# Kernel tuning notes

Measured on AMD Instinct MI355X. Metric: run time of the kernel, lower is better.

## Reference

```python
import jax, jax.numpy as jnp
import numpy as np

N_ENT = 14951   # entities (FB15K-style multimodal KG)
N_REL = 1345    # relations == number of context sub-graphs
N_NODES = 120000  # nodes in the batched context graph (b_x length)
N_EDGES = 480000  # edges in the normalized batched adjacency


def _glorot(key, shape):
    scale = np.sqrt(2.0 / (shape[0] + shape[1])).astype(np.float32)
    return jax.random.normal(key, shape, dtype=jnp.float32) * scale


def setup_inputs() -> dict:
    key = jax.random.key(0)
    ks = jax.random.split(key, 16)
    inp = {}
    inp["img_feat"] = jax.random.normal(ks[0], (N_ENT, 4096), dtype=jnp.float32)
    inp["text_feat"] = jax.random.normal(ks[1], (N_ENT, 300), dtype=jnp.float32)
    inp["rel_emb"] = jax.random.normal(ks[2], (N_REL, 300), dtype=jnp.float32)
    # learned parameters (eval mode: dropout = identity)
    inp["W_img_text"] = _glorot(ks[3], (4396, 100)); inp["b_img_text"] = jnp.zeros((100,), jnp.float32)
    inp["W_rel_input"] = _glorot(ks[4], (300, 100)); inp["b_rel_input"] = jnp.zeros((100,), jnp.float32)
    inp["W_gc1"] = _glorot(ks[5], (200, 256)); inp["b_gc1"] = jnp.zeros((256,), jnp.float32)
    inp["W_gc2"] = _glorot(ks[6], (256, 200)); inp["b_gc2"] = jnp.zeros((200,), jnp.float32)
    inp["W_emb"] = _glorot(ks[7], (400, 1)); inp["b_emb"] = jnp.zeros((1,), jnp.float32)
    inp["W_emb_out"] = _glorot(ks[8], (400, 200)); inp["b_emb_out"] = jnp.zeros((200,), jnp.float32)
    inp["W_rel"] = _glorot(ks[9], (300, 200)); inp["b_rel"] = jnp.zeros((200,), jnp.float32)
    # row-normalized adjacency of the batched context graph, as edge list
    inp["edge_weight"] = jax.random.uniform(ks[10], (N_EDGES,), dtype=jnp.float32)
    inp["b_x"] = jax.random.randint(ks[11], (N_NODES,), 0, N_ENT)
    inp["b_graph"] = jax.random.randint(ks[12], (N_NODES,), 0, N_REL)
    inp["edge_src"] = jax.random.randint(ks[13], (N_EDGES,), 0, N_NODES)
    inp["edge_dst"] = jax.random.randint(ks[14], (N_EDGES,), 0, N_NODES)
    return inp


def reference(img_feat, text_feat, rel_emb, W_img_text, b_img_text, W_rel_input,
              b_rel_input, W_gc1, b_gc1, W_gc2, b_gc2, W_emb, b_emb, W_emb_out,
              b_emb_out, W_rel, b_rel, edge_weight, b_x, b_graph, edge_src, edge_dst):
    seg_sum = lambda v, idx, n: jax.ops.segment_sum(v, idx, num_segments=n)

    def spmm(h):  # normalized adjacency @ h via edge-list gather/scatter
        return seg_sum(h[edge_src] * edge_weight[:, None], edge_dst, N_NODES)

    # multimodal entity encoder: Linear(4396 -> 100)
    emf = jnp.concatenate([img_feat, text_feat], axis=1) @ W_img_text + b_img_text
    # relation context encoder: Linear(300 -> 100) + ReLU
    rel_in = jax.nn.relu(rel_emb @ W_rel_input + b_rel_input)
    # batched context-graph node features [M, 200]
    h = jnp.concatenate([emf[b_x], rel_in[b_graph]], axis=1)
    # two-layer GCN encoder (SGCN1)
    h1 = jax.nn.relu(spmm(h @ W_gc1) + b_gc1)
    h2 = spmm(h1 @ W_gc2) + b_gc2          # [M, 200]
    # scatter_mean over entity ids, broadcast back
    cnt = seg_sum(jnp.ones((N_NODES,), h2.dtype), b_x, N_ENT)
    mean = seg_sum(h2, b_x, N_ENT) / jnp.maximum(cnt, 1.0)[:, None]
    emb = jnp.concatenate([h2, mean[b_x]], axis=1)   # [M, 400]
    score = emb @ W_emb + b_emb                      # [M, 1]
    # scatter_softmax over segments b_x (numerically stable)
    smax = jax.ops.segment_max(score, b_x, num_segments=N_ENT)
    e = jnp.exp(score - smax[b_x])
    z_s = e / seg_sum(e, b_x, N_ENT)[b_x]
    new_out = seg_sum(z_s * emb, b_x, N_ENT) @ W_emb_out + b_emb_out  # [N_ENT, 200]
    # relation output encoder: Linear(300 -> 200) + ReLU
    rel_context = jax.nn.relu(rel_emb @ W_rel + b_rel)                # [N_REL, 200]
    return new_out, rel_context
```

## Files before the change

kernel.cpp:

```cpp
#include <hip/hip_runtime.h>

#define N_ENT 14951
#define N_REL 1345
#define NNODE 120000
#define NEDGE 480000
#define MP_ENC 14976
#define KP_ENC 4480
#define NP_ENC 112

static inline int ceil_div(int a, int b){ return (a + b - 1) / b; }

typedef __bf16 bf16x8 __attribute__((ext_vector_type(8)));
typedef float f32x4 __attribute__((ext_vector_type(4)));

__device__ inline unsigned short f2bf(float f){
  unsigned u = __float_as_uint(f);
  return (unsigned short)((u + 0x7fffu + ((u >> 16) & 1u)) >> 16);
}

__global__ __launch_bounds__(256) void enc_mfma(
    const float* __restrict__ img, const float* __restrict__ txt,
    const unsigned short* __restrict__ Wt1, float* __restrict__ part)
{
  __shared__ unsigned short As[64 * 40];
  __shared__ unsigned short Bs[112 * 40];
  const int t = threadIdx.x;
  const int m0 = blockIdx.x * 64;
  const int s = blockIdx.y;
  const int l = t & 63, w = t >> 6;
  f32x4 acc[7];
  #pragma unroll
  for (int i = 0; i < 7; i++) acc[i] = f32x4{0.f, 0.f, 0.f, 0.f};

  for (int step = 0; step < 35; ++step) {
    const int kb = s * 1120 + step * 32;
    #pragma unroll
    for (int p = 0; p < 2; ++p) {
      const int c = t + p * 256;
      const int row = c >> 3, kq = c & 7;
      const int rowg = m0 + row;
      const int k = kb + kq * 4;
      float4 v = make_float4(0.f, 0.f, 0.f, 0.f);
      if (rowg < N_ENT) {
        if (k < 4096)      v = *(const float4*)(img + (size_t)rowg * 4096 + k);
        else if (k < 4396) v = *(const float4*)(txt + (size_t)rowg * 300 + (k - 4096));
      }
      ushort4 b;
      b.x = f2bf(v.x); b.y = f2bf(v.y); b.z = f2bf(v.z); b.w = f2bf(v.w);
      *(ushort4*)&As[row * 40 + kq * 4] = b;
    }
    {
      const int n = t >> 2, k16 = t & 3;
      *(uint4*)&Bs[n * 40 + k16 * 8] = *(const uint4*)(Wt1 + (size_t)n * KP_ENC + kb + k16 * 8);
      if (t < 192) {
        const int c = t + 256;
        const int n2 = c >> 2, k2 = c & 3;
        *(uint4*)&Bs[n2 * 40 + k2 * 8] = *(const uint4*)(Wt1 + (size_t)n2 * KP_ENC + kb + k2 * 8);
      }
    }
    __syncthreads();
    bf16x8 a = *(const bf16x8*)&As[(w * 16 + (l & 15)) * 40 + (l >> 4) * 8];
    #pragma unroll
    for (int ct = 0; ct < 7; ++ct) {
      bf16x8 bb = *(const bf16x8*)&Bs[(ct * 16 + (l & 15)) * 40 + (l >> 4) * 8];
      acc[ct] = __builtin_amdgcn_mfma_f32_16x16x32_bf16(a, bb, acc[ct], 0, 0, 0);
    }
    __syncthreads();
  }
  const int rb = m0 + w * 16 + (l >> 4) * 4;
  const int col = l & 15;
  #pragma unroll
  for (int ct = 0; ct < 7; ++ct)
    #pragma unroll
    for (int i = 0; i < 4; ++i)
      part[((size_t)s * MP_ENC + rb + i) * NP_ENC + ct * 16 + col] = acc[ct][i];
}

__global__ __launch_bounds__(256) void enc_reduce(
    const float* __restrict__ part, const float* __restrict__ bias, float* __restrict__ emf)
{
  int i = blockIdx.x * 256 + threadIdx.x;
  if (i >= N_ENT * 100) return;
  int r = i / 100, c = i % 100;
  float v = bias[c];
  #pragma unroll
  for (int s = 0; s < 4; ++s) v += part[((size_t)s * MP_ENC + r) * NP_ENC + c];
  emf[(size_t)r * 100 + c] = v;
}

__global__ __launch_bounds__(256) void gemm2_mfma(
    const float* __restrict__ h1, const unsigned short* __restrict__ Wt2,
    float* __restrict__ hg2)
{
  __shared__ unsigned short As[64 * 40];
  __shared__ unsigned short Bs[208 * 40];
  const int t = threadIdx.x;
  const int m0 = blockIdx.x * 64;
  const int l = t & 63, w = t >> 6;
  f32x4 acc[13];
  #pragma unroll
  for (int i = 0; i < 13; i++) acc[i] = f32x4{0.f, 0.f, 0.f, 0.f};

  for (int step = 0; step < 8; ++step) {
    const int kb = step * 32;
    #pragma unroll
    for (int p = 0; p < 2; ++p) {
      const int c = t + p * 256;
      const int row = c >> 3, kq = c & 7;
      float4 v = *(const float4*)(h1 + (size_t)(m0 + row) * 256 + kb + kq * 4);
      ushort4 b;
      b.x = f2bf(v.x); b.y = f2bf(v.y); b.z = f2bf(v.z); b.w = f2bf(v.w);
      *(ushort4*)&As[row * 40 + kq * 4] = b;
    }
    #pragma unroll
    for (int p = 0; p < 4; ++p) {
      const int c = t + p * 256;
      if (c < 832) {
        const int n = c >> 2, k16 = c & 3;
        *(uint4*)&Bs[n * 40 + k16 * 8] = *(const uint4*)(Wt2 + (size_t)n * 256 + kb + k16 * 8);
      }
    }
    __syncthreads();
    bf16x8 a = *(const bf16x8*)&As[(w * 16 + (l & 15)) * 40 + (l >> 4) * 8];
    #pragma unroll
    for (int ct = 0; ct < 13; ++ct) {
      bf16x8 bb = *(const bf16x8*)&Bs[(ct * 16 + (l & 15)) * 40 + (l >> 4) * 8];
      acc[ct] = __builtin_amdgcn_mfma_f32_16x16x32_bf16(a, bb, acc[ct], 0, 0, 0);
    }
    __syncthreads();
  }
  const int rb = m0 + w * 16 + (l >> 4) * 4;
  const int col0 = l & 15;
  #pragma unroll
  for (int ct = 0; ct < 13; ++ct) {
    const int col = ct * 16 + col0;
    if (col < 200) {
      #pragma unroll
      for (int i = 0; i < 4; ++i)
        hg2[(size_t)(rb + i) * 200 + col] = acc[ct][i];
    }
  }
}

__global__ __launch_bounds__(256) void wt1_k(const float* __restrict__ W, unsigned short* __restrict__ Wt)
{
  int n = blockIdx.y;
  int k = blockIdx.x * 256 + threadIdx.x;
  if (k >= KP_ENC) return;
  float v = (n < 100 && k < 4396) ? W[(size_t)k * 100 + n] : 0.f;
  Wt[(size_t)n * KP_ENC + k] = f2bf(v);
}
__global__ __launch_bounds__(256) void wt2_k(const float* __restrict__ W, unsigned short* __restrict__ Wt)
{
  int i = blockIdx.x * 256 + threadIdx.x;
  if (i >= 208 * 256) return;
  int n = i >> 8, k = i & 255;
  float v = (n < 200) ? W[(size_t)k * 200 + n] : 0.f;
  Wt[i] = f2bf(v);
}

template<bool RELU, bool HASBIAS>
__global__ __launch_bounds__(256) void gemm_f32(
    const float* __restrict__ A1, int K1, const float* __restrict__ A2,
    const float* __restrict__ B, const float* __restrict__ bias,
    float* __restrict__ C, int M, int K, int N)
{
  constexpr int BM = 64, BN = 128, BK = 16;
  __shared__ float As[BK][BM + 4];
  __shared__ float Bs[BK][BN];
  const int t = threadIdx.x;
  const int m0 = blockIdx.y * BM, n0 = blockIdx.x * BN;
  const int tr = t >> 4, tc = t & 15;
  const int tm0 = tr * 4, tn0 = tc * 8;
  const int K2 = K - K1;
  const int arow = t >> 2, aq = (t & 3) * 4;
  const int brow = t >> 4, bc0 = (t & 15) * 4;
  float acc[4][8];
  #pragma unroll
  for (int i = 0; i < 4; i++)
    #pragma unroll
    for (int j = 0; j < 8; j++) acc[i][j] = 0.f;

  for (int k0 = 0; k0 < K; k0 += BK) {
    {
      const int r = m0 + arow;
      const int k = k0 + aq;
      float4 v = make_float4(0.f, 0.f, 0.f, 0.f);
      if (r < M) {
        if (k + 3 < K1) {
          v = *(const float4*)(A1 + (size_t)r * K1 + k);
        } else if (k >= K1 && (k - K1) + 3 < K2) {
          v = *(const float4*)(A2 + (size_t)r * K2 + (k - K1));
        } else {
          float tmp[4] = {0.f, 0.f, 0.f, 0.f};
          #pragma unroll
          for (int j = 0; j < 4; j++) {
            int kj = k + j;
            if (kj < K) tmp[j] = (kj < K1) ? A1[(size_t)r * K1 + kj]
                                           : A2[(size_t)r * K2 + (kj - K1)];
          }
          v = make_float4(tmp[0], tmp[1], tmp[2], tmp[3]);
        }
      }
      As[aq + 0][arow] = v.x; As[aq + 1][arow] = v.y;
      As[aq + 2][arow] = v.z; As[aq + 3][arow] = v.w;
    }
    {
      const int k = k0 + brow;
      #pragma unroll
      for (int h = 0; h < 2; h++) {
        const int n = n0 + bc0 + h * 64;
        float4 v = make_float4(0.f, 0.f, 0.f, 0.f);
        if (k < K) {
          if (n + 3 < N) {
            v = *(const float4*)(B + (size_t)k * N + n);
          } else {
            float tmp[4] = {0.f, 0.f, 0.f, 0.f};
            for (int j = 0; j < 4; j++) if (n + j < N) tmp[j] = B[(size_t)k * N + n + j];
            v = make_float4(tmp[0], tmp[1], tmp[2], tmp[3]);
          }
        }
        *(float4*)&Bs[brow][bc0 + h * 64] = v;
      }
    }
    __syncthreads();
    #pragma unroll
    for (int k = 0; k < BK; k++) {
      float a[4], b[8];
      *(float4*)&a[0] = *(const float4*)&As[k][tm0];
      *(float4*)&b[0] = *(const float4*)&Bs[k][tn0];
      *(float4*)&b[4] = *(const float4*)&Bs[k][tn0 + 4];
      #pragma unroll
      for (int i = 0; i < 4; i++)
        #pragma unroll
        for (int j = 0; j < 8; j++) acc[i][j] = fmaf(a[i], b[j], acc[i][j]);
    }
    __syncthreads();
  }
  #pragma unroll
  for (int i = 0; i < 4; i++) {
    const int r = m0 + tm0 + i;
    if (r >= M) continue;
    #pragma unroll
    for (int j = 0; j < 8; j++) {
      const int c = n0 + tn0 + j;
      if (c >= N) continue;
      float v = acc[i][j];
      if (HASBIAS) v += bias[c];
      if (RELU) v = fmaxf(v, 0.f);
      C[(size_t)r * N + c] = v;
    }
  }
}

__global__ __launch_bounds__(256) void hist_k(const int* __restrict__ idx, int* __restrict__ hist, int n)
{
  int i = blockIdx.x * blockDim.x + threadIdx.x;
  if (i < n) atomicAdd(&hist[idx[i]], 1);
}

__global__ __launch_bounds__(256) void scan1_k(const int* __restrict__ hist, int* __restrict__ base,
                                               int* __restrict__ partial, int n)
{
  __shared__ int s[256];
  const int t = threadIdx.x;
  const int i0 = blockIdx.x * 1024 + t * 4;
  int v[4];
  #pragma unroll
  for (int j = 0; j < 4; j++) v[j] = (i0 + j < n) ? hist[i0 + j] : 0;
  const int tsum = v[0] + v[1] + v[2] + v[3];
  s[t] = tsum;
  __syncthreads();
  #pragma unroll
  for (int off = 1; off < 256; off <<= 1) {
    int u = (t >= off) ? s[t - off] : 0;
    __syncthreads();
    s[t] += u;
    __syncthreads();
  }
  int run = s[t] - tsum;
  #pragma unroll
  for (int j = 0; j < 4; j++) {
    if (i0 + j < n) base[i0 + j] = run;
    run += v[j];
  }
  if (t == 255) partial[blockIdx.x] = s[255];
}

__global__ __launch_bounds__(256) void scan2_k(int* __restrict__ partial, int nb, int* __restrict__ total_dst)
{
  __shared__ int s[256];
  const int t = threadIdx.x;
  const int v = (t < nb) ? partial[t] : 0;
  s[t] = v;
  __syncthreads();
  #pragma unroll
  for (int off = 1; off < 256; off <<= 1) {
    int u = (t >= off) ? s[t - off] : 0;
    __syncthreads();
    s[t] += u;
    __syncthreads();
  }
  if (t < nb) partial[t] = s[t] - v;
  if (t == 255) *total_dst = s[255];
}

__global__ __launch_bounds__(256) void scan3_k(int* __restrict__ base, const int* __restrict__ partial, int n)
{
  int i = blockIdx.x * 256 + threadIdx.x;
  if (i < n) base[i] += partial[blockIdx.x >> 2];
}

__global__ __launch_bounds__(256) void edge_scatter_k(
    const int* __restrict__ esrc, const int* __restrict__ edst, const float* __restrict__ ew,
    const int* __restrict__ bx, const int* __restrict__ bg,
    const int* __restrict__ ebase, int* __restrict__ ecur,
    float* __restrict__ s_w, int* __restrict__ s_src,
    int* __restrict__ s_en, int* __restrict__ s_gn)
{
  int e = blockIdx.x * blockDim.x + threadIdx.x;
  if (e >= NEDGE) return;
  int d = edst[e];
  int p = ebase[d] + atomicAdd(&ecur[d], 1);
  int s = esrc[e];
  s_w[p] = ew[e];
  s_src[p] = s;
  s_en[p] = bx[s];
  s_gn[p] = bg[s];
}

__global__ __launch_bounds__(256) void node_scatter_k(
    const int* __restrict__ bx, const int* __restrict__ nbase, int* __restrict__ ncur,
    int* __restrict__ node_of)
{
  int i = blockIdx.x * blockDim.x + threadIdx.x;
  if (i >= NNODE) return;
  int ent = bx[i];
  int p = nbase[ent] + atomicAdd(&ncur[ent], 1);
  node_of[p] = i;
}

__global__ __launch_bounds__(256) void spmm1_g(
    const int* __restrict__ ebase, const float* __restrict__ s_w,
    const int* __restrict__ s_en, const int* __restrict__ s_gn,
    const float* __restrict__ eg1, const float* __restrict__ rg1,
    const float* __restrict__ b_g1, float* __restrict__ out)
{
  const int gid = blockIdx.x * blockDim.x + threadIdx.x;
  const int d = gid >> 6, lane = gid & 63;
  if (d >= NNODE) return;
  const int p0 = ebase[d], p1 = ebase[d + 1];
  float4 acc = make_float4(0.f, 0.f, 0.f, 0.f);
  for (int p = p0; p < p1; ++p) {
    const float w = s_w[p];
    const int en = s_en[p], gn = s_gn[p];
    const float4 v = ((const float4*)(eg1 + (size_t)en * 256))[lane];
    const float4 u = ((const float4*)(rg1 + (size_t)gn * 256))[lane];
    acc.x += w * (v.x + u.x); acc.y += w * (v.y + u.y);
    acc.z += w * (v.z + u.z); acc.w += w * (v.w + u.w);
  }
  const float4 b = ((const float4*)b_g1)[lane];
  acc.x = fmaxf(acc.x + b.x, 0.f); acc.y = fmaxf(acc.y + b.y, 0.f);
  acc.z = fmaxf(acc.z + b.z, 0.f); acc.w = fmaxf(acc.w + b.w, 0.f);
  ((float4*)(out + (size_t)d * 256))[lane] = acc;
}

__global__ __launch_bounds__(256) void spmm2_g(
    const int* __restrict__ ebase, const float* __restrict__ s_w,
    const int* __restrict__ s_src, const float* __restrict__ hg2,
    const float* __restrict__ b_g2, const float* __restrict__ W_e,
    float* __restrict__ h2, float* __restrict__ score)
{
  const int gid = blockIdx.x * blockDim.x + threadIdx.x;
  const int d = gid >> 6, lane = gid & 63;
  if (d >= NNODE) return;
  const int p0 = ebase[d], p1 = ebase[d + 1];
  float4 acc = make_float4(0.f, 0.f, 0.f, 0.f);
  if (lane < 50) {
    for (int p = p0; p < p1; ++p) {
      const float w = s_w[p];
      const int s = s_src[p];
      const float4 v = ((const float4*)(hg2 + (size_t)s * 200))[lane];
      acc.x += w * v.x; acc.y += w * v.y; acc.z += w * v.z; acc.w += w * v.w;
    }
    const float4 b = ((const float4*)b_g2)[lane];
    acc.x += b.x; acc.y += b.y; acc.z += b.z; acc.w += b.w;
    ((float4*)(h2 + (size_t)d * 200))[lane] = acc;
  }
  float s = 0.f;
  if (lane < 50) {
    const float4 we = ((const float4*)W_e)[lane];
    s = acc.x * we.x + acc.y * we.y + acc.z * we.z + acc.w * we.w;
  }
  for (int off = 32; off; off >>= 1) s += __shfl_down(s, off);
  if (lane == 0) score[d] = s;
}

__global__ __launch_bounds__(256) void ent_k(
    const int* __restrict__ nbase, const int* __restrict__ node_of,
    const float* __restrict__ h2, const float* __restrict__ score,
    float* __restrict__ embE)
{
  const int gid = blockIdx.x * blockDim.x + threadIdx.x;
  const int ent = gid >> 6, lane = gid & 63;
  if (ent >= N_ENT) return;
  const int p0 = nbase[ent], p1 = nbase[ent + 1];
  const int cnt = p1 - p0;
  float m = -3.4e38f;
  for (int p = p0 + lane; p < p1; p += 64) m = fmaxf(m, score[node_of[p]]);
  #pragma unroll
  for (int off = 32; off; off >>= 1) m = fmaxf(m, __shfl_xor(m, off));
  float es = 0.f;
  for (int p = p0 + lane; p < p1; p += 64) es += __expf(score[node_of[p]] - m);
  #pragma unroll
  for (int off = 32; off; off >>= 1) es += __shfl_xor(es, off);
  const float inv_es = (cnt > 0) ? 1.f / es : 0.f;
  const float inv_cnt = 1.f / fmaxf((float)cnt, 1.f);
  float4 aw = make_float4(0.f, 0.f, 0.f, 0.f);
  float4 am = make_float4(0.f, 0.f, 0.f, 0.f);
  for (int p = p0; p < p1; ++p) {
    const int nd = node_of[p];
    const float z = __expf(score[nd] - m) * inv_es;
    if (lane < 50) {
      const float4 v = ((const float4*)(h2 + (size_t)nd * 200))[lane];
      aw.x += z * v.x; aw.y += z * v.y; aw.z += z * v.z; aw.w += z * v.w;
      am.x += v.x; am.y += v.y; am.z += v.z; am.w += v.w;
    }
  }
  if (lane < 50) {
    ((float4*)(embE + (size_t)ent * 400))[lane] = aw;
    float4 mn = make_float4(am.x * inv_cnt, am.y * inv_cnt, am.z * inv_cnt, am.w * inv_cnt);
    ((float4*)(embE + (size_t)ent * 400 + 200))[lane] = mn;
  }
}

extern "C" void kernel_launch(void* const* d_in, const int* in_sizes, int n_in,
                              void* d_out, int out_size, void* d_ws, size_t ws_size,
                              hipStream_t stream)
{
  const float* img  = (const float*)d_in[0];
  const float* txt  = (const float*)d_in[1];
  const float* rel  = (const float*)d_in[2];
  const float* W_it = (const float*)d_in[3];
  const float* b_it = (const float*)d_in[4];
  const float* W_ri = (const float*)d_in[5];
  const float* b_ri = (const float*)d_in[6];
  const float* W_g1 = (const float*)d_in[7];
  const float* b_g1 = (const float*)d_in[8];
  const float* W_g2 = (const float*)d_in[9];
  const float* b_g2 = (const float*)d_in[10];
  const float* W_e  = (const float*)d_in[11];
  const float* W_eo = (const float*)d_in[13];
  const float* b_eo = (const float*)d_in[14];
  const float* W_r  = (const float*)d_in[15];
  const float* b_r  = (const float*)d_in[16];
  const float* ew   = (const float*)d_in[17];
  const int*   bx   = (const int*)d_in[18];
  const int*   bg   = (const int*)d_in[19];
  const int*   esrc = (const int*)d_in[20];
  const int*   edst = (const int*)d_in[21];

  float* ws = (float*)d_ws;
  size_t off = 0;
  auto alloc = [&](size_t n){ size_t r = off; off += (n + 255) & ~(size_t)255; return r; };
  float* emf  = ws + alloc((size_t)N_ENT * 100);
  float* rin  = ws + alloc((size_t)N_REL * 100);
  float* eg1  = ws + alloc((size_t)N_ENT * 256);
  float* rg1  = ws + alloc((size_t)N_REL * 256);
  float* big1 = ws + alloc((size_t)NNODE * 256);
  float* hg2  = ws + alloc((size_t)NNODE * 200);
  float* embE = ws + alloc((size_t)N_ENT * 400);
  float* score = ws + alloc(NNODE);
  int* ehist = (int*)(ws + alloc(NNODE));
  int* ecur  = (int*)(ws + alloc(NNODE));
  int* ebase = (int*)(ws + alloc(NNODE + 1));
  int* nhist = (int*)(ws + alloc(N_ENT));
  int* ncur  = (int*)(ws + alloc(N_ENT));
  int* nbase = (int*)(ws + alloc(N_ENT + 1));
  int* epart = (int*)(ws + alloc(256));
  int* npart = (int*)(ws + alloc(256));
  float* s_w  = ws + alloc(NEDGE);
  int* s_src  = (int*)(ws + alloc(NEDGE));
  int* s_en   = (int*)(ws + alloc(NEDGE));
  int* s_gn   = (int*)(ws + alloc(NEDGE));
  int* node_of = (int*)(ws + alloc(NNODE));
  unsigned short* Wt1 = (unsigned short*)(ws + alloc((size_t)NP_ENC * KP_ENC / 2));
  unsigned short* Wt2 = (unsigned short*)(ws + alloc((size_t)208 * 256 / 2));
  float* part = hg2;
  float* h2 = big1;

  dim3 blk(256);

  hipMemsetAsync(ehist, 0, (size_t)NNODE * 4, stream);
  hipMemsetAsync(ecur,  0, (size_t)NNODE * 4, stream);
  hipMemsetAsync(nhist, 0, (size_t)N_ENT * 4, stream);
  hipMemsetAsync(ncur,  0, (size_t)N_ENT * 4, stream);
  hist_k<<<ceil_div(NEDGE, 256), blk, 0, stream>>>(edst, ehist, NEDGE);
  hist_k<<<ceil_div(NNODE, 256), blk, 0, stream>>>(bx, nhist, NNODE);
  scan1_k<<<ceil_div(NNODE, 1024), blk, 0, stream>>>(ehist, ebase, epart, NNODE);
  scan2_k<<<1, blk, 0, stream>>>(epart, ceil_div(NNODE, 1024), ebase + NNODE);
  scan3_k<<<ceil_div(NNODE, 256), blk, 0, stream>>>(ebase, epart, NNODE);
  scan1_k<<<ceil_div(N_ENT, 1024), blk, 0, stream>>>(nhist, nbase, npart, N_ENT);
  scan2_k<<<1, blk, 0, stream>>>(npart, ceil_div(N_ENT, 1024), nbase + N_ENT);
  scan3_k<<<ceil_div(N_ENT, 256), blk, 0, stream>>>(nbase, npart, N_ENT);
  edge_scatter_k<<<ceil_div(NEDGE, 256), blk, 0, stream>>>(
      esrc, edst, ew, bx, bg, ebase, ecur, s_w, s_src, s_en, s_gn);
  node_scatter_k<<<ceil_div(NNODE, 256), blk, 0, stream>>>(bx, nbase, ncur, node_of);

  wt1_k<<<dim3(ceil_div(KP_ENC, 256), NP_ENC), blk, 0, stream>>>(W_it, Wt1);
  wt2_k<<<ceil_div(208 * 256, 256), blk, 0, stream>>>(W_g2, Wt2);

  enc_mfma<<<dim3(MP_ENC / 64, 4), blk, 0, stream>>>(img, txt, Wt1, part);
  enc_reduce<<<ceil_div(N_ENT * 100, 256), blk, 0, stream>>>(part, b_it, emf);

  gemm_f32<true, true><<<dim3(1, ceil_div(N_REL, 64)), blk, 0, stream>>>(
      rel, 300, rel, W_ri, b_ri, rin, N_REL, 300, 100);
  gemm_f32<false, false><<<dim3(2, ceil_div(N_ENT, 64)), blk, 0, stream>>>(
      emf, 100, emf, W_g1, nullptr, eg1, N_ENT, 100, 256);
  gemm_f32<false, false><<<dim3(2, ceil_div(N_REL, 64)), blk, 0, stream>>>(
      rin, 100, rin, W_g1 + 100 * 256, nullptr, rg1, N_REL, 100, 256);

  spmm1_g<<<ceil_div(NNODE * 64, 256), blk, 0, stream>>>(
      ebase, s_w, s_en, s_gn, eg1, rg1, b_g1, big1);

  gemm2_mfma<<<NNODE / 64, blk, 0, stream>>>(big1, Wt2, hg2);
  spmm2_g<<<ceil_div(NNODE * 64, 256), blk, 0, stream>>>(
      ebase, s_w, s_src, hg2, b_g2, W_e, h2, score);

  ent_k<<<ceil_div(N_ENT * 64, 256), blk, 0, stream>>>(nbase, node_of, h2, score, embE);

  float* out_new = (float*)d_out;
  float* out_rel = out_new + (size_t)N_ENT * 200;
  gemm_f32<false, true><<<dim3(2, ceil_div(N_ENT, 64)), blk, 0, stream>>>(
      embE, 400, embE, W_eo, b_eo, out_new, N_ENT, 400, 200);
  gemm_f32<true, true><<<dim3(2, ceil_div(N_REL, 64)), blk, 0, stream>>>(
      rel, 300, rel, W_r, b_r, out_rel, N_REL, 300, 200);
}
```

Before: 706.6 us.

## Reorder GCN layers to aggregate before transform and fuse score into GEMM

Both GCN layers now do the sparse neighbour aggregation first and the dense weight multiply second, instead of the reverse. Layer 1 gathers the narrow 100-wide entity and relation features and then runs a new bf16 MFMA GEMM with fused bias and ReLU. This replaces the fp32 per-entity GEMMs and the 512-float-per-edge gathers. Layer 2 gathers the 256-wide h1 rows and then runs the MFMA GEMM with fused bias and the attention-score dot product. The cost is a wider random gather in layer 2 and an extra full-size intermediate buffer, and layer-1 inputs are now rounded to bf16 after aggregation.

```diff
diff --git a/kernel.cpp b/kernel.cpp
--- a/kernel.cpp
+++ b/kernel.cpp
@@ -88,9 +88,61 @@
   emf[(size_t)r * 100 + c] = v;
 }
 
-__global__ __launch_bounds__(256) void gemm2_mfma(
-    const float* __restrict__ h1, const unsigned short* __restrict__ Wt2,
-    float* __restrict__ hg2)
+__global__ __launch_bounds__(256) void gemm1_mfma(
+    const float* __restrict__ hagg, const unsigned short* __restrict__ Wtg1,
+    const float* __restrict__ b_g1, float* __restrict__ h1)
+{
+  __shared__ unsigned short As[64 * 40];
+  __shared__ unsigned short Bs[256 * 40];
+  const int t = threadIdx.x;
+  const int m0 = blockIdx.x * 64;
+  const int l = t & 63, w = t >> 6;
+  f32x4 acc[16];
+  #pragma unroll
+  for (int i = 0; i < 16; i++) acc[i] = f32x4{0.f, 0.f, 0.f, 0.f};
+
+  for (int step = 0; step < 7; ++step) {
+    const int kb = step * 32;
+    #pragma unroll
+    for (int p = 0; p < 2; ++p) {
+      const int c = t + p * 256;
+      const int row = c >> 3, kq = c & 7;
+      float4 v = *(const float4*)(hagg + (size_t)(m0 + row) * 224 + kb + kq * 4);
+      ushort4 b;
+      b.x = f2bf(v.x); b.y = f2bf(v.y); b.z = f2bf(v.z); b.w = f2bf(v.w);
+      *(ushort4*)&As[row * 40 + kq * 4] = b;
+    }
+    #pragma unroll
+    for (int p = 0; p < 4; ++p) {
+      const int c = t + p * 256;
+      const int n = c >> 2, k16 = c & 3;
+      *(uint4*)&Bs[n * 40 + k16 * 8] = *(const uint4*)(Wtg1 + (size_t)n * 224 + kb + k16 * 8);
+    }
+    __syncthreads();
+    bf16x8 a = *(const bf16x8*)&As[(w * 16 + (l & 15)) * 40 + (l >> 4) * 8];
+    #pragma unroll
+    for (int ct = 0; ct < 16; ++ct) {
+      bf16x8 bb = *(const bf16x8*)&Bs[(ct * 16 + (l & 15)) * 40 + (l >> 4) * 8];
+      acc[ct] = __builtin_amdgcn_mfma_f32_16x16x32_bf16(a, bb, acc[ct], 0, 0, 0);
+    }
+    __syncthreads();
+  }
+  const int rb = m0 + w * 16 + (l >> 4) * 4;
+  const int col0 = l & 15;
+  #pragma unroll
+  for (int ct = 0; ct < 16; ++ct) {
+    const int col = ct * 16 + col0;
+    const float b = b_g1[col];
+    #pragma unroll
+    for (int i = 0; i < 4; ++i)
+      h1[(size_t)(rb + i) * 256 + col] = fmaxf(acc[ct][i] + b, 0.f);
+  }
+}
+
+__global__ __launch_bounds__(256) void gemm2s_mfma(
+    const float* __restrict__ hagg2, const unsigned short* __restrict__ Wt2,
+    const float* __restrict__ b_g2, const float* __restrict__ W_e,
+    float* __restrict__ h2, float* __restrict__ score)
 {
   __shared__ unsigned short As[64 * 40];
   __shared__ unsigned short Bs[208 * 40];
@@ -107,7 +159,7 @@
     for (int p = 0; p < 2; ++p) {
       const int c = t + p * 256;
       const int row = c >> 3, kq = c & 7;
-      float4 v = *(const float4*)(h1 + (size_t)(m0 + row) * 256 + kb + kq * 4);
+      float4 v = *(const float4*)(hagg2 + (size_t)(m0 + row) * 256 + kb + kq * 4);
       ushort4 b;
       b.x = f2bf(v.x); b.y = f2bf(v.y); b.z = f2bf(v.z); b.w = f2bf(v.w);
       *(ushort4*)&As[row * 40 + kq * 4] = b;
@@ -131,14 +183,29 @@
   }
   const int rb = m0 + w * 16 + (l >> 4) * 4;
   const int col0 = l & 15;
+  float sp[4] = {0.f, 0.f, 0.f, 0.f};
   #pragma unroll
   for (int ct = 0; ct < 13; ++ct) {
     const int col = ct * 16 + col0;
     if (col < 200) {
+      const float b = b_g2[col];
+      const float we = W_e[col];
       #pragma unroll
-      for (int i = 0; i < 4; ++i)
-        hg2[(size_t)(rb + i) * 200 + col] = acc[ct][i];
-    }
+      for (int i = 0; i < 4; ++i) {
+        const float v = acc[ct][i] + b;
+        h2[(size_t)(rb + i) * 200 + col] = v;
+        sp[i] += v * we;
+      }
+    }
+  }
+  #pragma unroll
+  for (int m = 1; m < 16; m <<= 1) {
+    #pragma unroll
+    for (int i = 0; i < 4; ++i) sp[i] += __shfl_xor(sp[i], m);
+  }
+  if ((l & 15) == 0) {
+    #pragma unroll
+    for (int i = 0; i < 4; ++i) score[rb + i] = sp[i];
   }
 }
 
@@ -149,6 +216,14 @@
   if (k >= KP_ENC) return;
   float v = (n < 100 && k < 4396) ? W[(size_t)k * 100 + n] : 0.f;
   Wt[(size_t)n * KP_ENC + k] = f2bf(v);
+}
+__global__ __launch_bounds__(256) void wtg1_k(const float* __restrict__ W, unsigned short* __restrict__ Wt)
+{
+  int i = blockIdx.x * 256 + threadIdx.x;
+  if (i >= 256 * 224) return;
+  int n = i / 224, k = i % 224;
+  float v = (k < 200) ? W[(size_t)k * 256 + n] : 0.f;
+  Wt[i] = f2bf(v);
 }
 __global__ __launch_bounds__(256) void wt2_k(const float* __restrict__ W, unsigned short* __restrict__ Wt)
 {
@@ -340,11 +415,37 @@
   node_of[p] = i;
 }
 
-__global__ __launch_bounds__(256) void spmm1_g(
+__global__ __launch_bounds__(256) void hagg1_k(
     const int* __restrict__ ebase, const float* __restrict__ s_w,
     const int* __restrict__ s_en, const int* __restrict__ s_gn,
-    const float* __restrict__ eg1, const float* __restrict__ rg1,
-    const float* __restrict__ b_g1, float* __restrict__ out)
+    const float* __restrict__ emf, const float* __restrict__ rin,
+    float* __restrict__ hagg)
+{
+  const int gid = blockIdx.x * blockDim.x + threadIdx.x;
+  const int d = gid >> 6, lane = gid & 63;
+  if (d >= NNODE) return;
+  const int p0 = ebase[d], p1 = ebase[d + 1];
+  float4 acc = make_float4(0.f, 0.f, 0.f, 0.f);
+  if (lane < 25) {
+    for (int p = p0; p < p1; ++p) {
+      const float w = s_w[p];
+      const float4 v = ((const float4*)(emf + (size_t)s_en[p] * 100))[lane];
+      acc.x += w * v.x; acc.y += w * v.y; acc.z += w * v.z; acc.w += w * v.w;
+    }
+  } else if (lane < 50) {
+    for (int p = p0; p < p1; ++p) {
+      const float w = s_w[p];
+      const float4 v = ((const float4*)(rin + (size_t)s_gn[p] * 100))[lane - 25];
+      acc.x += w * v.x; acc.y += w * v.y; acc.z += w * v.z; acc.w += w * v.w;
+    }
+  }
+  if (lane < 56) ((float4*)(hagg + (size_t)d * 224))[lane] = acc;
+}
+
+__global__ __launch_bounds__(256) void hagg2_k(
+    const int* __restrict__ ebase, const float* __restrict__ s_w,
+    const int* __restrict__ s_src, const float* __restrict__ h1,
+    float* __restrict__ hagg2)
 {
   const int gid = blockIdx.x * blockDim.x + threadIdx.x;
   const int d = gid >> 6, lane = gid & 63;
@@ -353,47 +454,10 @@
   float4 acc = make_float4(0.f, 0.f, 0.f, 0.f);
   for (int p = p0; p < p1; ++p) {
     const float w = s_w[p];
-    const int en = s_en[p], gn = s_gn[p];
-    const float4 v = ((const float4*)(eg1 + (size_t)en * 256))[lane];
-    const float4 u = ((const float4*)(rg1 + (size_t)gn * 256))[lane];
-    acc.x += w * (v.x + u.x); acc.y += w * (v.y + u.y);
-    acc.z += w * (v.z + u.z); acc.w += w * (v.w + u.w);
-  }
-  const float4 b = ((const float4*)b_g1)[lane];
-  acc.x = fmaxf(acc.x + b.x, 0.f); acc.y = fmaxf(acc.y + b.y, 0.f);
-  acc.z = fmaxf(acc.z + b.z, 0.f); acc.w = fmaxf(acc.w + b.w, 0.f);
-  ((float4*)(out + (size_t)d * 256))[lane] = acc;
-}
-
-__global__ __launch_bounds__(256) void spmm2_g(
-    const int* __restrict__ ebase, const float* __restrict__ s_w,
-    const int* __restrict__ s_src, const float* __restrict__ hg2,
-    const float* __restrict__ b_g2, const float* __restrict__ W_e,
-    float* __restrict__ h2, float* __restrict__ score)
-{
-  const int gid = blockIdx.x * blockDim.x + threadIdx.x;
-  const int d = gid >> 6, lane = gid & 63;
-  if (d >= NNODE) return;
-  const int p0 = ebase[d], p1 = ebase[d + 1];
-  float4 acc = make_float4(0.f, 0.f, 0.f, 0.f);
-  if (lane < 50) {
-    for (int p = p0; p < p1; ++p) {
-      const float w = s_w[p];
-      const int s = s_src[p];
-      const float4 v = ((const float4*)(hg2 + (size_t)s * 200))[lane];
-      acc.x += w * v.x; acc.y += w * v.y; acc.z += w * v.z; acc.w += w * v.w;
-    }
-    const float4 b = ((const float4*)b_g2)[lane];
-    acc.x += b.x; acc.y += b.y; acc.z += b.z; acc.w += b.w;
-    ((float4*)(h2 + (size_t)d * 200))[lane] = acc;
-  }
-  float s = 0.f;
-  if (lane < 50) {
-    const float4 we = ((const float4*)W_e)[lane];
-    s = acc.x * we.x + acc.y * we.y + acc.z * we.z + acc.w * we.w;
-  }
-  for (int off = 32; off; off >>= 1) s += __shfl_down(s, off);
-  if (lane == 0) score[d] = s;
+    const float4 v = ((const float4*)(h1 + (size_t)s_src[p] * 256))[lane];
+    acc.x += w * v.x; acc.y += w * v.y; acc.z += w * v.z; acc.w += w * v.w;
+  }
+  ((float4*)(hagg2 + (size_t)d * 256))[lane] = acc;
 }
 
 __global__ __launch_bounds__(256) void ent_k(
@@ -463,13 +527,12 @@
   float* ws = (float*)d_ws;
   size_t off = 0;
   auto alloc = [&](size_t n){ size_t r = off; off += (n + 255) & ~(size_t)255; return r; };
-  float* emf  = ws + alloc((size_t)N_ENT * 100);
-  float* rin  = ws + alloc((size_t)N_REL * 100);
-  float* eg1  = ws + alloc((size_t)N_ENT * 256);
-  float* rg1  = ws + alloc((size_t)N_REL * 256);
-  float* big1 = ws + alloc((size_t)NNODE * 256);
-  float* hg2  = ws + alloc((size_t)NNODE * 200);
-  float* embE = ws + alloc((size_t)N_ENT * 400);
+  float* emf   = ws + alloc((size_t)N_ENT * 100);
+  float* rin   = ws + alloc((size_t)N_REL * 100);
+  float* big1  = ws + alloc((size_t)NNODE * 256);
+  float* hagg1 = ws + alloc((size_t)NNODE * 224);
+  float* hagg2 = ws + alloc((size_t)NNODE * 256);
+  float* embE  = ws + alloc((size_t)N_ENT * 400);
   float* score = ws + alloc(NNODE);
   int* ehist = (int*)(ws + alloc(NNODE));
   int* ecur  = (int*)(ws + alloc(NNODE));
@@ -484,9 +547,10 @@
   int* s_en   = (int*)(ws + alloc(NEDGE));
   int* s_gn   = (int*)(ws + alloc(NEDGE));
   int* node_of = (int*)(ws + alloc(NNODE));
-  unsigned short* Wt1 = (unsigned short*)(ws + alloc((size_t)NP_ENC * KP_ENC / 2));
-  unsigned short* Wt2 = (unsigned short*)(ws + alloc((size_t)208 * 256 / 2));
-  float* part = hg2;
+  unsigned short* Wt1  = (unsigned short*)(ws + alloc((size_t)NP_ENC * KP_ENC / 2));
+  unsigned short* Wtg1 = (unsigned short*)(ws + alloc((size_t)256 * 224 / 2));
+  unsigned short* Wt2  = (unsigned short*)(ws + alloc((size_t)208 * 256 / 2));
+  float* part = hagg1;
   float* h2 = big1;
 
   dim3 blk(256);
@@ -508,24 +572,21 @@
   node_scatter_k<<<ceil_div(NNODE, 256), blk, 0, stream>>>(bx, nbase, ncur, node_of);
 
   wt1_k<<<dim3(ceil_div(KP_ENC, 256), NP_ENC), blk, 0, stream>>>(W_it, Wt1);
+  wtg1_k<<<ceil_div(256 * 224, 256), blk, 0, stream>>>(W_g1, Wtg1);
   wt2_k<<<ceil_div(208 * 256, 256), blk, 0, stream>>>(W_g2, Wt2);
 
   enc_mfma<<<dim3(MP_ENC / 64, 4), blk, 0, stream>>>(img, txt, Wt1, part);
   enc_reduce<<<ceil_div(N_ENT * 100, 256), blk, 0, stream>>>(part, b_it, emf);
-
   gemm_f32<true, true><<<dim3(1, ceil_div(N_REL, 64)), blk, 0, stream>>>(
       rel, 300, rel, W_ri, b_ri, rin, N_REL, 300, 100);
-  gemm_f32<false, false><<<dim3(2, ceil_div(N_ENT, 64)), blk, 0, stream>>>(
-      emf, 100, emf, W_g1, nullptr, eg1, N_ENT, 100, 256);
-  gemm_f32<false, false><<<dim3(2, ceil_div(N_REL, 64)), blk, 0, stream>>>(
-      rin, 100, rin, W_g1 + 100 * 256, nullptr, rg1, N_REL, 100, 256);
-
-  spmm1_g<<<ceil_div(NNODE * 64, 256), blk, 0, stream>>>(
-      ebase, s_w, s_en, s_gn, eg1, rg1, b_g1, big1);
-
-  gemm2_mfma<<<NNODE / 64, blk, 0, stream>>>(big1, Wt2, hg2);
-  spmm2_g<<<ceil_div(NNODE * 64, 256), blk, 0, stream>>>(
-      ebase, s_w, s_src, hg2, b_g2, W_e, h2, score);
+
+  hagg1_k<<<ceil_div(NNODE * 64, 256), blk, 0, stream>>>(
+      ebase, s_w, s_en, s_gn, emf, rin, hagg1);
+  gemm1_mfma<<<NNODE / 64, blk, 0, stream>>>(hagg1, Wtg1, b_g1, big1);
+
+  hagg2_k<<<ceil_div(NNODE * 64, 256), blk, 0, stream>>>(
+      ebase, s_w, s_src, big1, hagg2);
+  gemm2s_mfma<<<NNODE / 64, blk, 0, stream>>>(hagg2, Wt2, b_g2, W_e, h2, score);
 
   ent_k<<<ceil_div(N_ENT * 64, 256), blk, 0, stream>>>(nbase, node_of, h2, score, embE);
 
```

Result: slower. 736.6 us (+4.2%).
